# Optimization experiments

Measured on AMD Instinct MI355X. Metric: run time of the kernel, lower is better.

## Reference

```python
import jax, jax.numpy as jnp
import numpy as np

NUM_HEADS = 8

def setup_inputs() -> dict:
    key = jax.random.key(0)
    ks = jax.random.split(key, 8)
    B, L, S, D = 4, 2048, 2048, 256
    q = jax.random.normal(ks[0], (B, L, D), dtype=jnp.float32)
    k = jax.random.normal(ks[1], (B, S, D), dtype=jnp.float32)
    self_other_mask = jax.random.bernoulli(ks[2], 0.5, (B, L, S))
    mask = jnp.zeros((B, L, S), dtype=jnp.float32)
    # xavier-uniform-like linear weights (torch Linear weight is [out, in])
    lim = float(np.sqrt(6.0 / (D + D)))
    def w(kk):
        return jax.random.uniform(kk, (D, D), dtype=jnp.float32, minval=-lim, maxval=lim)
    return {
        'q': q, 'k': k, 'self_other_mask': self_other_mask, 'mask': mask,
        'Wq_self': w(ks[3]), 'Wq_other': w(ks[4]),
        'Wk_self': w(ks[5]), 'Wk_other': w(ks[6]),
    }


def reference(q, k, self_other_mask, mask, Wq_self, Wq_other, Wk_self, Wk_other):
    B, L, D = q.shape
    S = k.shape[1]
    H = NUM_HEADS
    hd = D // H
    scale = hd ** -0.5  # qk_scaling
    # projections (torch Linear: x @ W.T), scale applied to queries
    q_self = (q @ Wq_self.T) * scale
    q_other = (q @ Wq_other.T) * scale
    k_self = k @ Wk_self.T
    k_other = k @ Wk_other.T
    # split heads: [B, L, H, hd]
    q_self = q_self.reshape(B, L, H, hd)
    q_other = q_other.reshape(B, L, H, hd)
    k_self = k_self.reshape(B, S, H, hd)
    k_other = k_other.reshape(B, S, H, hd)
    # scores: [B, H, L, S]
    att_self = jnp.einsum('blhd,bshd->bhls', q_self, k_self)
    att_other = jnp.einsum('blhd,bshd->bhls', q_other, k_other)
    # blend by self/other mask (broadcast over heads), then additive mask
    som = self_other_mask[:, None, :, :]  # [B,1,L,S]
    attention = jnp.where(som, att_self, att_other) + mask[:, None, :, :]
    return attention
```

## Files before the change

### kernel.cpp

```cpp
#include <hip/hip_runtime.h>
#include <hip/hip_bf16.h>


typedef __attribute__((ext_vector_type(8))) __bf16 bf16x8;
typedef __attribute__((ext_vector_type(4))) float f32x4;
typedef __attribute__((ext_vector_type(4))) int i32x4;

#define MFMA16(a, b, c) __builtin_amdgcn_mfma_f32_16x16x32_bf16((a), (b), (c), 0, 0, 0)

__device__ __forceinline__ bf16x8 load8_f32_to_bf16(const float* __restrict__ p) {
    float4 f0 = *(const float4*)p;
    float4 f1 = *(const float4*)(p + 4);
    bf16x8 r;
    r[0] = (__bf16)f0.x; r[1] = (__bf16)f0.y; r[2] = (__bf16)f0.z; r[3] = (__bf16)f0.w;
    r[4] = (__bf16)f1.x; r[5] = (__bf16)f1.y; r[6] = (__bf16)f1.z; r[7] = (__bf16)f1.w;
    return r;
}

__global__ __launch_bounds__(256) void proj_kernel(
    const float* __restrict__ qin, const float* __restrict__ kin,
    const float* __restrict__ Wqs, const float* __restrict__ Wqo,
    const float* __restrict__ Wks, const float* __restrict__ Wko,
    __bf16* __restrict__ qout, __bf16* __restrict__ kout)
{
    const bool isK = blockIdx.y >= 64;
    const float* in = isK ? kin : qin;
    const float* Ws = isK ? Wks : Wqs;
    const float* Wo = isK ? Wko : Wqo;
    __bf16* outp    = isK ? kout : qout;
    const float scale = isK ? 1.0f : 0.17677669529663687f;

    const int n0 = blockIdx.x * 64;
    const int m0 = (blockIdx.y & 63) * 128;
    const int tid  = threadIdx.x;
    const int lane = tid & 63;
    const int w    = tid >> 6;
    const int wr = w >> 1, wc = w & 1;
    const int l15 = lane & 15, l4 = lane >> 4;

    f32x4 acc[4][2];
#pragma unroll
    for (int mi = 0; mi < 4; ++mi)
#pragma unroll
        for (int ni = 0; ni < 2; ++ni) acc[mi][ni] = (f32x4){0.f, 0.f, 0.f, 0.f};

    const int arow0 = m0 + wr * 64 + l15;

    const float* wptr[2];
#pragma unroll
    for (int ni = 0; ni < 2; ++ni) {
        int c = n0 + wc * 32 + ni * 16 + l15;
        wptr[ni] = (c < 256) ? (Ws + c * 256) : (Wo + (c - 256) * 256);
    }

#pragma unroll
    for (int ks = 0; ks < 8; ++ks) {
        const int k0 = ks * 32 + l4 * 8;
        bf16x8 a[4], b[2];
#pragma unroll
        for (int mi = 0; mi < 4; ++mi)
            a[mi] = load8_f32_to_bf16(in + (arow0 + mi * 16) * 256 + k0);
#pragma unroll
        for (int ni = 0; ni < 2; ++ni)
            b[ni] = load8_f32_to_bf16(wptr[ni] + k0);
#pragma unroll
        for (int mi = 0; mi < 4; ++mi)
#pragma unroll
            for (int ni = 0; ni < 2; ++ni)
                acc[mi][ni] = MFMA16(a[mi], b[ni], acc[mi][ni]);
    }

#pragma unroll
    for (int mi = 0; mi < 4; ++mi)
#pragma unroll
        for (int ni = 0; ni < 2; ++ni)
#pragma unroll
            for (int j = 0; j < 4; ++j) {
                int row = m0 + wr * 64 + mi * 16 + l4 * 4 + j;
                int col = n0 + wc * 32 + ni * 16 + l15;
                outp[row * 512 + col] = (__bf16)(acc[mi][ni][j] * scale);
            }
}

__global__ __launch_bounds__(256) void attn_kernel(
    const __bf16* __restrict__ qp, const __bf16* __restrict__ kp,
    const int* __restrict__ som, const float* __restrict__ mask,
    float* __restrict__ out)
{
    __shared__ float tile[128][68];

    const int s0 = blockIdx.x * 64;
    const int l0 = blockIdx.y * 128;
    const int b  = blockIdx.z;
    const int tid  = threadIdx.x;
    const int lane = tid & 63;
    const int w    = tid >> 6;
    const int l15 = lane & 15, l4 = lane >> 4;

    const int lrow0 = l0 + w * 32 + l15;
    const int scol0 = s0 + l4 * 4;

    f32x4 mreg[2][4];
    unsigned int sbits = 0;
#pragma unroll
    for (int mi = 0; mi < 2; ++mi)
#pragma unroll
        for (int ni = 0; ni < 4; ++ni) {
            int idx = (b * 2048 + lrow0 + mi * 16) * 2048 + scol0 + ni * 16;
            f32x4 m  = __builtin_nontemporal_load((const f32x4*)(mask + idx));
            i32x4 sm = __builtin_nontemporal_load((const i32x4*)(som + idx));
            mreg[mi][ni] = m;
            const int t0 = (mi * 4 + ni) * 4;
#pragma unroll
            for (int j = 0; j < 4; ++j)
                sbits |= (sm[j] != 0) ? (1u << (t0 + j)) : 0u;
        }

    const __bf16* qbase = qp + (b * 2048 + lrow0) * 512 + l4 * 8;
    const __bf16* kbase = kp + (b * 2048 + s0 + l15) * 512 + l4 * 8;

    const int lds_r0 = w * 32 + l15;
    const int lds_c0 = l4 * 4;

    const int st_row = tid >> 4;
    const int st_col = (tid & 15) * 4;

    for (int h = 0; h < 8; ++h) {
        const int hofs = h * 32;
        bf16x8 qb[2][2], ka[4][2];
#pragma unroll
        for (int mi = 0; mi < 2; ++mi)
#pragma unroll
            for (int p = 0; p < 2; ++p)
                qb[mi][p] = *(const bf16x8*)(qbase + mi * 16 * 512 + p * 256 + hofs);
#pragma unroll
        for (int ni = 0; ni < 4; ++ni)
#pragma unroll
            for (int p = 0; p < 2; ++p)
                ka[ni][p] = *(const bf16x8*)(kbase + ni * 16 * 512 + p * 256 + hofs);

#pragma unroll
        for (int mi = 0; mi < 2; ++mi)
#pragma unroll
            for (int ni = 0; ni < 4; ++ni) {
                f32x4 z = (f32x4){0.f, 0.f, 0.f, 0.f};
                f32x4 as = MFMA16(ka[ni][0], qb[mi][0], z);
                f32x4 ao = MFMA16(ka[ni][1], qb[mi][1], z);
                const int t0 = (mi * 4 + ni) * 4;
                f32x4 v;
#pragma unroll
                for (int j = 0; j < 4; ++j)
                    v[j] = (((sbits >> (t0 + j)) & 1u) ? as[j] : ao[j]) + mreg[mi][ni][j];
                *(f32x4*)&tile[lds_r0 + mi * 16][lds_c0 + ni * 16] = v;
            }

        __syncthreads();

        const long obase = ((long)(b * 8 + h) * 2048 + l0) * 2048 + s0;
#pragma unroll
        for (int p = 0; p < 8; ++p) {
            int r = p * 16 + st_row;
            f32x4 v = *(const f32x4*)&tile[r][st_col];
            *(f32x4*)(out + obase + (long)r * 2048 + st_col) = v;
        }

        __syncthreads();
    }
}

extern "C" void kernel_launch(void* const* d_in, const int* in_sizes, int n_in,
                              void* d_out, int out_size, void* d_ws, size_t ws_size,
                              hipStream_t stream) {
    const float* q    = (const float*)d_in[0];
    const float* k    = (const float*)d_in[1];
    const int*   som  = (const int*)d_in[2];
    const float* mask = (const float*)d_in[3];
    const float* Wqs  = (const float*)d_in[4];
    const float* Wqo  = (const float*)d_in[5];
    const float* Wks  = (const float*)d_in[6];
    const float* Wko  = (const float*)d_in[7];
    float* out = (float*)d_out;

    __bf16* qp = (__bf16*)d_ws;
    __bf16* kp = qp + 8192 * 512;

    dim3 pgrid(8, 128, 1), pblk(256, 1, 1);
    hipLaunchKernelGGL(proj_kernel, pgrid, pblk, 0, stream,
                       q, k, Wqs, Wqo, Wks, Wko, qp, kp);

    dim3 agrid(32, 16, 4), ablk(256, 1, 1);
    hipLaunchKernelGGL(attn_kernel, agrid, ablk, 0, stream, qp, kp, som, mask, out);
}
```

Baseline: 238.9 us.

## Reshape attention tile to 32x256 and stage mask/som loads through LDS

Changes the attention block tile from 128 L-rows by 64 S-columns to 32 rows by 256 columns, so each wave covers a 64-column slice across all 32 rows. The mask and self/other-mask reads now go row-contiguous (1KB per wave per row) into LDS and are redistributed to the MFMA layout, replacing scattered 16-byte loads. Output stores also become full 1KB row segments. The cost is extra LDS round trips and barriers before the head loop, and K rows are no longer shared across as many L rows, so Q/K reuse per block changes.

```diff
diff --git a/kernel.cpp b/kernel.cpp
--- a/kernel.cpp
+++ b/kernel.cpp
@@ -87,43 +87,57 @@
     const int* __restrict__ som, const float* __restrict__ mask,
     float* __restrict__ out)
 {
-    __shared__ float tile[128][68];
-
-    const int s0 = blockIdx.x * 64;
-    const int l0 = blockIdx.y * 128;
+    __shared__ float tile[32][260];
+
+    const int s0 = blockIdx.x * 256;
+    const int l0 = blockIdx.y * 32;
     const int b  = blockIdx.z;
     const int tid  = threadIdx.x;
     const int lane = tid & 63;
     const int w    = tid >> 6;
     const int l15 = lane & 15, l4 = lane >> 4;
 
-    const int lrow0 = l0 + w * 32 + l15;
-    const int scol0 = s0 + l4 * 4;
+    const int c_row = l15;
+    const int c_col = w * 64 + l4 * 4;
 
     f32x4 mreg[2][4];
     unsigned int sbits = 0;
 #pragma unroll
+    for (int i = 0; i < 8; ++i) {
+        int r = i * 4 + w;
+        f32x4 m = __builtin_nontemporal_load(
+            (const f32x4*)(mask + (long)(b * 2048 + l0 + r) * 2048 + s0 + 4 * lane));
+        *(f32x4*)&tile[r][4 * lane] = m;
+    }
+    __syncthreads();
+#pragma unroll
     for (int mi = 0; mi < 2; ++mi)
 #pragma unroll
+        for (int ni = 0; ni < 4; ++ni)
+            mreg[mi][ni] = *(const f32x4*)&tile[c_row + mi * 16][c_col + ni * 16];
+    __syncthreads();
+#pragma unroll
+    for (int i = 0; i < 8; ++i) {
+        int r = i * 4 + w;
+        i32x4 sm = __builtin_nontemporal_load(
+            (const i32x4*)(som + (long)(b * 2048 + l0 + r) * 2048 + s0 + 4 * lane));
+        *(i32x4*)&tile[r][4 * lane] = sm;
+    }
+    __syncthreads();
+#pragma unroll
+    for (int mi = 0; mi < 2; ++mi)
+#pragma unroll
         for (int ni = 0; ni < 4; ++ni) {
-            int idx = (b * 2048 + lrow0 + mi * 16) * 2048 + scol0 + ni * 16;
-            f32x4 m  = __builtin_nontemporal_load((const f32x4*)(mask + idx));
-            i32x4 sm = __builtin_nontemporal_load((const i32x4*)(som + idx));
-            mreg[mi][ni] = m;
+            i32x4 sm = *(const i32x4*)&tile[c_row + mi * 16][c_col + ni * 16];
             const int t0 = (mi * 4 + ni) * 4;
 #pragma unroll
             for (int j = 0; j < 4; ++j)
                 sbits |= (sm[j] != 0) ? (1u << (t0 + j)) : 0u;
         }
-
-    const __bf16* qbase = qp + (b * 2048 + lrow0) * 512 + l4 * 8;
-    const __bf16* kbase = kp + (b * 2048 + s0 + l15) * 512 + l4 * 8;
-
-    const int lds_r0 = w * 32 + l15;
-    const int lds_c0 = l4 * 4;
-
-    const int st_row = tid >> 4;
-    const int st_col = (tid & 15) * 4;
+    __syncthreads();
+
+    const __bf16* qbase = qp + (long)(b * 2048 + l0 + l15) * 512 + l4 * 8;
+    const __bf16* kbase = kp + (long)(b * 2048 + s0 + w * 64 + l15) * 512 + l4 * 8;
 
     for (int h = 0; h < 8; ++h) {
         const int hofs = h * 32;
@@ -151,17 +165,17 @@
 #pragma unroll
                 for (int j = 0; j < 4; ++j)
                     v[j] = (((sbits >> (t0 + j)) & 1u) ? as[j] : ao[j]) + mreg[mi][ni][j];
-                *(f32x4*)&tile[lds_r0 + mi * 16][lds_c0 + ni * 16] = v;
+                *(f32x4*)&tile[c_row + mi * 16][c_col + ni * 16] = v;
             }
 
         __syncthreads();
 
-        const long obase = ((long)(b * 8 + h) * 2048 + l0) * 2048 + s0;
-#pragma unroll
-        for (int p = 0; p < 8; ++p) {
-            int r = p * 16 + st_row;
-            f32x4 v = *(const f32x4*)&tile[r][st_col];
-            *(f32x4*)(out + obase + (long)r * 2048 + st_col) = v;
+        const long obase = (long)((b * 8 + h) * 2048 + l0) * 2048 + s0;
+#pragma unroll
+        for (int i = 0; i < 8; ++i) {
+            int r = i * 4 + w;
+            f32x4 v = *(const f32x4*)&tile[r][4 * lane];
+            *(f32x4*)(out + obase + (long)r * 2048 + 4 * lane) = v;
         }
 
         __syncthreads();
@@ -188,6 +202,6 @@
     hipLaunchKernelGGL(proj_kernel, pgrid, pblk, 0, stream,
                        q, k, Wqs, Wqo, Wks, Wko, qp, kp);
 
-    dim3 agrid(32, 16, 4), ablk(256, 1, 1);
+    dim3 agrid(8, 64, 4), ablk(256, 1, 1);
     hipLaunchKernelGGL(attn_kernel, agrid, ablk, 0, stream, qp, kp, som, mask, out);
 }
```

After: 203.7 us. 1.17x faster.
